# Kernel tuning notes

Hardware: AMD Instinct MI355X
Metric: run time of the kernel (lower is better)

The kernel has to match this reference:

```python
import jax, jax.numpy as jnp
import numpy as np

N, D, K = 50000, 512, 32  # n_nodes, dim_in, max neighbors (padded ragged edge_dict)


def setup_inputs() -> dict:
    key = jax.random.key(0)
    k1, k2, k3, k4, k5, k6, k7 = jax.random.split(key, 7)
    feats = jax.random.normal(k1, (N, D), dtype=jnp.float32)
    neighbors = jax.random.randint(k2, (N, K), 0, N)          # padded neighbor ids
    deg = jax.random.randint(k3, (N,), 0, K + 1)               # valid neighbor count (0 == leaf node branch)
    s = 1.0 / np.sqrt(D)  # torch nn.Linear default init range
    wq_w = jax.random.uniform(k4, (D,), jnp.float32, -s, s)
    wq_b = jax.random.uniform(k5, (), jnp.float32, -s, s)
    wk_w = jax.random.uniform(k6, (D,), jnp.float32, -s, s)
    wk_b = jax.random.uniform(k7, (), jnp.float32, -s, s)
    return dict(feats=feats, wq_w=wq_w, wq_b=wq_b, wk_w=wk_w, wk_b=wk_b,
                neighbors=neighbors, deg=deg)


def reference(feats, wq_w, wq_b, wk_w, wk_b, neighbors, deg):
    # Faithful to the original: feats is updated IN PLACE node-by-node, so later
    # nodes read already-updated neighbor features -> sequential lax.scan.
    arange_k = jnp.arange(neighbors.shape[1])
    NEG = jnp.float32(-1e9)

    def step(f, inp):
        i, nbr, d = inp
        mask = (arange_k < d).astype(f.dtype)      # [K] valid-neighbor mask
        nb = f[nbr]                                 # [K, D] neighbor gather
        ei = jnp.dot(f[i], wq_w) + wq_b             # scalar: w_q(center)
        ej = nb @ wk_w + wk_b                       # [K]:    w_k(neighbors)
        eij = ei * ej
        a = jax.nn.softmax(jnp.where(mask > 0, eij, NEG)) * mask  # softmax over dim 0
        upd = a @ nb                                # [D] weighted sum (zero when deg==0)
        new = f[i] + upd                            # in-place add_ on center row
        f = f.at[i].set(new)
        return f, new

    _, rows = jax.lax.scan(step, feats, (jnp.arange(feats.shape[0]), neighbors, deg))
    # Original returns torch.LongTensor(edge_feats) (a lossy int cast of the updated
    # rows); we return the float rows, which carry the actual computed math.
    return rows
```

## Files before the change

kernel.cpp:

```cpp
#include <hip/hip_runtime.h>


constexpr int NN = 50000;
constexpr int D  = 512;
constexpr int K  = 32;
constexpr int D4 = D / 4;

typedef float v4f __attribute__((ext_vector_type(4)));

__device__ __forceinline__ void store_f4_llc(float* p, float4 v) {
    v4f vv; vv.x = v.x; vv.y = v.y; vv.z = v.z; vv.w = v.w;
    asm volatile("global_store_dwordx4 %0, %1, off sc0 sc1"
                 :: "v"(p), "v"(vv) : "memory");
}

__global__ __launch_bounds__(256) void precomp_kernel(
    const float* __restrict__ feats,
    const float* __restrict__ wq_w, const float* __restrict__ wq_b,
    const float* __restrict__ wk_w, const float* __restrict__ wk_b,
    float* __restrict__ ei, float* __restrict__ ej_orig)
{
    int gw   = (int)((blockIdx.x * blockDim.x + threadIdx.x) >> 6);
    int lane = threadIdx.x & 63;
    if (gw >= NN) return;
    const float4* row = (const float4*)feats + (size_t)gw * D4;
    const float4* q4  = (const float4*)wq_w;
    const float4* k4  = (const float4*)wk_w;
    float dq = 0.f, dk = 0.f;
#pragma unroll
    for (int c = 0; c < 2; ++c) {
        float4 v  = row[lane + 64 * c];
        float4 q  = q4[lane + 64 * c];
        float4 kk = k4[lane + 64 * c];
        dq += v.x * q.x + v.y * q.y + v.z * q.z + v.w * q.w;
        dk += v.x * kk.x + v.y * kk.y + v.z * kk.z + v.w * kk.w;
    }
#pragma unroll
    for (int off = 32; off > 0; off >>= 1) {
        dq += __shfl_down(dq, off, 64);
        dk += __shfl_down(dk, off, 64);
    }
    if (lane == 0) {
        ei[gw]      = dq + wq_b[0];
        ej_orig[gw] = dk + wk_b[0];
    }
}

__global__ __launch_bounds__(256, 4) void attn_dataflow(
    const float* __restrict__ feats,
    const int* __restrict__ neighbors, const int* __restrict__ deg,
    const float* __restrict__ ei_arr, const float* __restrict__ ej_orig,
    const float* __restrict__ wk_w, const float* __restrict__ wk_b,
    int* ej_new,
    float* out)
{
    const int lane   = threadIdx.x & 63;
    const int gwave  = (int)((blockIdx.x * blockDim.x + threadIdx.x) >> 6);
    const int nwaves = (int)((gridDim.x * blockDim.x) >> 6);
    const float4* f4  = (const float4*)feats;
    const float4* o4r = (const float4*)out;
    const float4* wk4 = (const float4*)wk_w;
    const float   wkb = wk_b[0];

    for (int id = gwave; id < NN; id += nwaves) {
        const int d = deg[id];
        int nbr = 0;
        if (lane < K) nbr = neighbors[(size_t)id * K + lane];
        const bool valid = lane < d;
        const bool isdep = valid && (nbr < id);

        const float4 c0 = f4[(size_t)id * D4 + lane];
        const float4 c1 = f4[(size_t)id * D4 + lane + 64];
        const float eii = ei_arr[id];

        float eij = 0.f;
        if (valid && !isdep) eij = eii * ej_orig[nbr];

        float4 acc0 = {0.f, 0.f, 0.f, 0.f};
        float4 acc1 = {0.f, 0.f, 0.f, 0.f};
        float m = -3.0e38f, s = 0.f;

        unsigned long long pend = __ballot(valid && !isdep);
        unsigned long long wait = __ballot(isdep);

        while (pend | wait) {
            if (!pend) {
                int pv = 0;
                const bool w = (wait >> lane) & 1ULL;
                if (w) pv = __hip_atomic_load(&ej_new[nbr], __ATOMIC_RELAXED,
                                              __HIP_MEMORY_SCOPE_AGENT);
                unsigned long long ready = __ballot(w && pv != 0);
                if (!ready) { __builtin_amdgcn_s_sleep(1); continue; }
                if (w && pv != 0) eij = eii * __int_as_float(pv);
                pend = ready;
                wait &= ~ready;
            }
            int cnt = 0;
            int   js[4]; float ee[4];
#pragma unroll
            for (int t = 0; t < 4; ++t) {
                if (pend) {
                    int k = (int)__ffsll(pend) - 1;
                    pend &= pend - 1;
                    ee[cnt] = __shfl(eij, k, 64);
                    js[cnt] = __shfl(nbr, k, 64);
                    ++cnt;
                }
            }
            float4 v0[4], v1[4];
#pragma unroll
            for (int t = 0; t < 4; ++t) {
                if (t < cnt) {
                    const float4* sp = (js[t] < id) ? (o4r + (size_t)js[t] * D4)
                                                    : (f4  + (size_t)js[t] * D4);
                    v0[t] = sp[lane];
                    v1[t] = sp[lane + 64];
                }
            }
            float mb = m;
#pragma unroll
            for (int t = 0; t < 4; ++t) if (t < cnt) mb = fmaxf(mb, ee[t]);
            if (mb > m) {
                const float r = __expf(m - mb);
                acc0.x *= r; acc0.y *= r; acc0.z *= r; acc0.w *= r;
                acc1.x *= r; acc1.y *= r; acc1.z *= r; acc1.w *= r;
                s *= r; m = mb;
            }
#pragma unroll
            for (int t = 0; t < 4; ++t) {
                if (t < cnt) {
                    const float wt = __expf(ee[t] - m);
                    s += wt;
                    acc0.x += wt * v0[t].x; acc0.y += wt * v0[t].y;
                    acc0.z += wt * v0[t].z; acc0.w += wt * v0[t].w;
                    acc1.x += wt * v1[t].x; acc1.y += wt * v1[t].y;
                    acc1.z += wt * v1[t].z; acc1.w += wt * v1[t].w;
                }
            }
        }

        const float inv_s = (s > 0.f) ? (1.0f / s) : 0.f;
        float4 g0 = {c0.x + acc0.x * inv_s, c0.y + acc0.y * inv_s,
                     c0.z + acc0.z * inv_s, c0.w + acc0.w * inv_s};
        float4 g1 = {c1.x + acc1.x * inv_s, c1.y + acc1.y * inv_s,
                     c1.z + acc1.z * inv_s, c1.w + acc1.w * inv_s};
        float* orow = out + (size_t)id * D;
        store_f4_llc(orow + 4 * lane,        g0);
        store_f4_llc(orow + 4 * (lane + 64), g1);

        float4 w0 = wk4[lane], w1 = wk4[lane + 64];
        float pd = g0.x * w0.x + g0.y * w0.y + g0.z * w0.z + g0.w * w0.w
                 + g1.x * w1.x + g1.y * w1.y + g1.z * w1.z + g1.w * w1.w;
#pragma unroll
        for (int off = 32; off > 0; off >>= 1)
            pd += __shfl_xor(pd, off, 64);

        int bits = __float_as_int(pd + wkb);
        if (bits == 0) bits = 1;

        __builtin_amdgcn_s_waitcnt(0);
        if (lane == 0)
            __hip_atomic_store(&ej_new[id], bits,
                               __ATOMIC_RELAXED, __HIP_MEMORY_SCOPE_AGENT);
    }
}

extern "C" void kernel_launch(void* const* d_in, const int* in_sizes, int n_in,
                              void* d_out, int out_size, void* d_ws, size_t ws_size,
                              hipStream_t stream)
{
    const float* feats     = (const float*)d_in[0];
    const float* wq_w      = (const float*)d_in[1];
    const float* wq_b      = (const float*)d_in[2];
    const float* wk_w      = (const float*)d_in[3];
    const float* wk_b      = (const float*)d_in[4];
    const int*   neighbors = (const int*)d_in[5];
    const int*   deg       = (const int*)d_in[6];
    float*       out       = (float*)d_out;

    char*  ws      = (char*)d_ws;
    int*   ej_new  = (int*)ws;
    float* ei      = (float*)(ws + (size_t)(NN + 128) * sizeof(int));
    float* ej_orig = ei + NN;

    (void)hipMemsetAsync(d_ws, 0, (size_t)(NN + 128) * sizeof(int), stream);

    dim3 pb(256), pg((NN + 3) / 4);
    precomp_kernel<<<pg, pb, 0, stream>>>(feats, wq_w, wq_b, wk_w, wk_b, ei, ej_orig);

    attn_dataflow<<<dim3(1024), dim3(256), 0, stream>>>(
        feats, neighbors, deg, ei, ej_orig, wk_w, wk_b, ej_new, out);
}
```

Before: 427.9 us.

## Fuse projection precompute into dataflow kernel with per-node readiness flags

Drops the separate precompute kernel. Each wave first computes the q/k projections for its own nodes, then publishes the k projection through a flag array that consumers poll, just as they already poll updated neighbors. This removes the kernel boundary and the grid-wide wait between precompute and the sequential attention pass, so the two stages can overlap. It also doubles the grid and raises the occupancy hint to 8 blocks per CU. In exchange, every neighbor now needs a polling step, and correctness depends on all 2048 blocks being resident at once to avoid spin-wait deadlock.

After: 568.4 us. +32.8%, slower.

```diff
diff --git a/kernel.cpp b/kernel.cpp
--- a/kernel.cpp
+++ b/kernel.cpp
@@ -14,44 +14,12 @@
                  :: "v"(p), "v"(vv) : "memory");
 }
 
-__global__ __launch_bounds__(256) void precomp_kernel(
+__global__ __launch_bounds__(256, 8) void attn_dataflow(
     const float* __restrict__ feats,
+    const int* __restrict__ neighbors, const int* __restrict__ deg,
     const float* __restrict__ wq_w, const float* __restrict__ wq_b,
     const float* __restrict__ wk_w, const float* __restrict__ wk_b,
-    float* __restrict__ ei, float* __restrict__ ej_orig)
-{
-    int gw   = (int)((blockIdx.x * blockDim.x + threadIdx.x) >> 6);
-    int lane = threadIdx.x & 63;
-    if (gw >= NN) return;
-    const float4* row = (const float4*)feats + (size_t)gw * D4;
-    const float4* q4  = (const float4*)wq_w;
-    const float4* k4  = (const float4*)wk_w;
-    float dq = 0.f, dk = 0.f;
-#pragma unroll
-    for (int c = 0; c < 2; ++c) {
-        float4 v  = row[lane + 64 * c];
-        float4 q  = q4[lane + 64 * c];
-        float4 kk = k4[lane + 64 * c];
-        dq += v.x * q.x + v.y * q.y + v.z * q.z + v.w * q.w;
-        dk += v.x * kk.x + v.y * kk.y + v.z * kk.z + v.w * kk.w;
-    }
-#pragma unroll
-    for (int off = 32; off > 0; off >>= 1) {
-        dq += __shfl_down(dq, off, 64);
-        dk += __shfl_down(dk, off, 64);
-    }
-    if (lane == 0) {
-        ei[gw]      = dq + wq_b[0];
-        ej_orig[gw] = dk + wk_b[0];
-    }
-}
-
-__global__ __launch_bounds__(256, 4) void attn_dataflow(
-    const float* __restrict__ feats,
-    const int* __restrict__ neighbors, const int* __restrict__ deg,
-    const float* __restrict__ ei_arr, const float* __restrict__ ej_orig,
-    const float* __restrict__ wk_w, const float* __restrict__ wk_b,
-    int* ej_new,
+    int* ej_new, int* ej_orig, float* ei_arr,
     float* out)
 {
     const int lane   = threadIdx.x & 63;
@@ -59,8 +27,33 @@
     const int nwaves = (int)((gridDim.x * blockDim.x) >> 6);
     const float4* f4  = (const float4*)feats;
     const float4* o4r = (const float4*)out;
+    const float4* wq4 = (const float4*)wq_w;
     const float4* wk4 = (const float4*)wk_w;
+    const float   wqb = wq_b[0];
     const float   wkb = wk_b[0];
+
+    for (int id = gwave; id < NN; id += nwaves) {
+        const float4* row = f4 + (size_t)id * D4;
+        float4 v0 = row[lane],      v1 = row[lane + 64];
+        float4 q0 = wq4[lane],      q1 = wq4[lane + 64];
+        float4 k0 = wk4[lane],      k1 = wk4[lane + 64];
+        float dq = v0.x*q0.x + v0.y*q0.y + v0.z*q0.z + v0.w*q0.w
+                 + v1.x*q1.x + v1.y*q1.y + v1.z*q1.z + v1.w*q1.w;
+        float dk = v0.x*k0.x + v0.y*k0.y + v0.z*k0.z + v0.w*k0.w
+                 + v1.x*k1.x + v1.y*k1.y + v1.z*k1.z + v1.w*k1.w;
+#pragma unroll
+        for (int off = 32; off > 0; off >>= 1) {
+            dq += __shfl_down(dq, off, 64);
+            dk += __shfl_down(dk, off, 64);
+        }
+        if (lane == 0) {
+            ei_arr[id] = dq + wqb;
+            int b = __float_as_int(dk + wkb);
+            if (b == 0) b = 1;
+            __hip_atomic_store(&ej_orig[id], b,
+                               __ATOMIC_RELAXED, __HIP_MEMORY_SCOPE_AGENT);
+        }
+    }
 
     for (int id = gwave; id < NN; id += nwaves) {
         const int d = deg[id];
@@ -68,26 +61,25 @@
         if (lane < K) nbr = neighbors[(size_t)id * K + lane];
         const bool valid = lane < d;
         const bool isdep = valid && (nbr < id);
+        const int* watch = isdep ? ej_new : ej_orig;
 
         const float4 c0 = f4[(size_t)id * D4 + lane];
         const float4 c1 = f4[(size_t)id * D4 + lane + 64];
         const float eii = ei_arr[id];
 
         float eij = 0.f;
-        if (valid && !isdep) eij = eii * ej_orig[nbr];
-
         float4 acc0 = {0.f, 0.f, 0.f, 0.f};
         float4 acc1 = {0.f, 0.f, 0.f, 0.f};
         float m = -3.0e38f, s = 0.f;
 
-        unsigned long long pend = __ballot(valid && !isdep);
-        unsigned long long wait = __ballot(isdep);
+        unsigned long long pend = 0;
+        unsigned long long wait = __ballot(valid);
 
         while (pend | wait) {
             if (!pend) {
                 int pv = 0;
                 const bool w = (wait >> lane) & 1ULL;
-                if (w) pv = __hip_atomic_load(&ej_new[nbr], __ATOMIC_RELAXED,
+                if (w) pv = __hip_atomic_load(&watch[nbr], __ATOMIC_RELAXED,
                                               __HIP_MEMORY_SCOPE_AGENT);
                 unsigned long long ready = __ballot(w && pv != 0);
                 if (!ready) { __builtin_amdgcn_s_sleep(1); continue; }
@@ -180,14 +172,11 @@
 
     char*  ws      = (char*)d_ws;
     int*   ej_new  = (int*)ws;
-    float* ei      = (float*)(ws + (size_t)(NN + 128) * sizeof(int));
-    float* ej_orig = ei + NN;
+    int*   ej_orig = ej_new + NN + 64;
+    float* ei      = (float*)(ej_orig + NN + 64);
 
-    (void)hipMemsetAsync(d_ws, 0, (size_t)(NN + 128) * sizeof(int), stream);
+    (void)hipMemsetAsync(d_ws, 0, (size_t)(2 * NN + 128) * sizeof(int), stream);
 
-    dim3 pb(256), pg((NN + 3) / 4);
-    precomp_kernel<<<pg, pb, 0, stream>>>(feats, wq_w, wq_b, wk_w, wk_b, ei, ej_orig);
-
-    attn_dataflow<<<dim3(1024), dim3(256), 0, stream>>>(
-        feats, neighbors, deg, ei, ej_orig, wk_w, wk_b, ej_new, out);
+    attn_dataflow<<<dim3(2048), dim3(256), 0, stream>>>(
+        feats, neighbors, deg, wq_w, wq_b, wk_w, wk_b, ej_new, ej_orig, ei, out);
 }
```

## Gather neighbor rows from fp16 shadow copies and batch eight neighbors per step

Applied to the files above, without the earlier changes.

The precompute kernel now also writes an fp16 copy of the input features. The main kernel keeps an fp16 shadow of each updated output row alongside the fp32 output. Neighbor gathers read these half-precision rows, which halves the bytes moved on the dependent critical path, and the batch size grows from four to eight neighbors per loop iteration with padded lanes. This costs accuracy in the weighted sum and an extra 100MB of workspace writes, and falls back to the fp32 path when the workspace is too small.

New measurement: 366.8 us. 14.3% less time.

```diff
diff --git a/kernel.cpp b/kernel.cpp
--- a/kernel.cpp
+++ b/kernel.cpp
@@ -1,24 +1,40 @@
 #include <hip/hip_runtime.h>
-
-
-constexpr int NN = 50000;
-constexpr int D  = 512;
-constexpr int K  = 32;
-constexpr int D4 = D / 4;
-
-typedef float v4f __attribute__((ext_vector_type(4)));
+#include <hip/hip_fp16.h>
+
+
+constexpr int NN   = 50000;
+constexpr int D    = 512;
+constexpr int K    = 32;
+constexpr int D4   = D / 4;
+constexpr int DU16 = D / 2;
+
+typedef float        v4f __attribute__((ext_vector_type(4)));
+typedef unsigned int v4u __attribute__((ext_vector_type(4)));
 
 __device__ __forceinline__ void store_f4_llc(float* p, float4 v) {
     v4f vv; vv.x = v.x; vv.y = v.y; vv.z = v.z; vv.w = v.w;
     asm volatile("global_store_dwordx4 %0, %1, off sc0 sc1"
                  :: "v"(p), "v"(vv) : "memory");
 }
+__device__ __forceinline__ void store_u4_llc(unsigned int* p, v4u v) {
+    asm volatile("global_store_dwordx4 %0, %1, off sc0 sc1"
+                 :: "v"(p), "v"(v) : "memory");
+}
+__device__ __forceinline__ unsigned int packh2(float a, float b) {
+    __half2 h = __floats2half2_rn(a, b);
+    return *reinterpret_cast<unsigned int*>(&h);
+}
+__device__ __forceinline__ float2 unpackh2(unsigned int u) {
+    __half2 h = *reinterpret_cast<__half2*>(&u);
+    return __half22float2(h);
+}
 
 __global__ __launch_bounds__(256) void precomp_kernel(
     const float* __restrict__ feats,
     const float* __restrict__ wq_w, const float* __restrict__ wq_b,
     const float* __restrict__ wk_w, const float* __restrict__ wk_b,
-    float* __restrict__ ei, float* __restrict__ ej_orig)
+    float* __restrict__ ei, float* __restrict__ ej_orig,
+    unsigned int* __restrict__ feats16)
 {
     int gw   = (int)((blockIdx.x * blockDim.x + threadIdx.x) >> 6);
     int lane = threadIdx.x & 63;
@@ -26,33 +42,156 @@
     const float4* row = (const float4*)feats + (size_t)gw * D4;
     const float4* q4  = (const float4*)wq_w;
     const float4* k4  = (const float4*)wk_w;
-    float dq = 0.f, dk = 0.f;
-#pragma unroll
-    for (int c = 0; c < 2; ++c) {
-        float4 v  = row[lane + 64 * c];
-        float4 q  = q4[lane + 64 * c];
-        float4 kk = k4[lane + 64 * c];
-        dq += v.x * q.x + v.y * q.y + v.z * q.z + v.w * q.w;
-        dk += v.x * kk.x + v.y * kk.y + v.z * kk.z + v.w * kk.w;
-    }
+    float4 v0 = row[2 * lane], v1 = row[2 * lane + 1];
+    float4 q0 = q4[2 * lane],  q1 = q4[2 * lane + 1];
+    float4 k0 = k4[2 * lane],  k1 = k4[2 * lane + 1];
+    float dq = v0.x*q0.x + v0.y*q0.y + v0.z*q0.z + v0.w*q0.w
+             + v1.x*q1.x + v1.y*q1.y + v1.z*q1.z + v1.w*q1.w;
+    float dk = v0.x*k0.x + v0.y*k0.y + v0.z*k0.z + v0.w*k0.w
+             + v1.x*k1.x + v1.y*k1.y + v1.z*k1.z + v1.w*k1.w;
 #pragma unroll
     for (int off = 32; off > 0; off >>= 1) {
         dq += __shfl_down(dq, off, 64);
         dk += __shfl_down(dk, off, 64);
     }
+    if (feats16) {
+        v4u p;
+        p.x = packh2(v0.x, v0.y); p.y = packh2(v0.z, v0.w);
+        p.z = packh2(v1.x, v1.y); p.w = packh2(v1.z, v1.w);
+        *(v4u*)(feats16 + (size_t)gw * DU16 + 4 * lane) = p;
+    }
     if (lane == 0) {
         ei[gw]      = dq + wq_b[0];
         ej_orig[gw] = dk + wk_b[0];
     }
 }
 
-__global__ __launch_bounds__(256, 4) void attn_dataflow(
+__global__ __launch_bounds__(256, 4) void attn_dataflow_h16(
     const float* __restrict__ feats,
     const int* __restrict__ neighbors, const int* __restrict__ deg,
     const float* __restrict__ ei_arr, const float* __restrict__ ej_orig,
     const float* __restrict__ wk_w, const float* __restrict__ wk_b,
-    int* ej_new,
-    float* out)
+    const unsigned int* __restrict__ feats16, unsigned int* __restrict__ out16,
+    int* ej_new, float* out)
+{
+    const int lane   = threadIdx.x & 63;
+    const int gwave  = (int)((blockIdx.x * blockDim.x + threadIdx.x) >> 6);
+    const int nwaves = (int)((gridDim.x * blockDim.x) >> 6);
+    const float4* f4  = (const float4*)feats;
+    const float4* wk4 = (const float4*)wk_w;
+    const float   wkb = wk_b[0];
+
+    for (int id = gwave; id < NN; id += nwaves) {
+        const int d = deg[id];
+        int nbr = 0;
+        if (lane < K) nbr = neighbors[(size_t)id * K + lane];
+        const bool valid = lane < d;
+        const bool isdep = valid && (nbr < id);
+
+        const float4 c0 = f4[(size_t)id * D4 + 2 * lane];
+        const float4 c1 = f4[(size_t)id * D4 + 2 * lane + 1];
+        const float eii = ei_arr[id];
+
+        float eij = 0.f;
+        if (valid && !isdep) eij = eii * ej_orig[nbr];
+
+        float4 acc0 = {0.f, 0.f, 0.f, 0.f};
+        float4 acc1 = {0.f, 0.f, 0.f, 0.f};
+        float m = -3.0e38f, s = 0.f;
+
+        unsigned long long pend = __ballot(valid && !isdep);
+        unsigned long long wait = __ballot(isdep);
+
+        while (pend | wait) {
+            if (!pend) {
+                int pv = 0;
+                const bool w = (wait >> lane) & 1ULL;
+                if (w) pv = __hip_atomic_load(&ej_new[nbr], __ATOMIC_RELAXED,
+                                              __HIP_MEMORY_SCOPE_AGENT);
+                unsigned long long ready = __ballot(w && pv != 0);
+                if (!ready) { __builtin_amdgcn_s_sleep(1); continue; }
+                if (w && pv != 0) eij = eii * __int_as_float(pv);
+                pend = ready;
+                wait &= ~ready;
+            }
+            int js_[8]; float ee[8]; int klast = 0;
+#pragma unroll
+            for (int t = 0; t < 8; ++t) {
+                const bool has = (pend != 0);
+                int k = has ? ((int)__ffsll(pend) - 1) : klast;
+                if (has) pend &= pend - 1;
+                klast = k;
+                float ev = __shfl(eij, k, 64);
+                ee[t] = has ? ev : -3.0e38f;
+                js_[t] = __shfl(nbr, k, 64);
+            }
+            v4u pv8[8];
+#pragma unroll
+            for (int t = 0; t < 8; ++t) {
+                const unsigned int* sp = ((js_[t] < id) ? out16 : feats16)
+                                         + (size_t)js_[t] * DU16 + 4 * lane;
+                pv8[t] = *(const v4u*)sp;
+            }
+            float mb = m;
+#pragma unroll
+            for (int t = 0; t < 8; ++t) mb = fmaxf(mb, ee[t]);
+            if (mb > m) {
+                const float r = __expf(m - mb);
+                acc0.x *= r; acc0.y *= r; acc0.z *= r; acc0.w *= r;
+                acc1.x *= r; acc1.y *= r; acc1.z *= r; acc1.w *= r;
+                s *= r; m = mb;
+            }
+#pragma unroll
+            for (int t = 0; t < 8; ++t) {
+                const float wt = __expf(ee[t] - m);
+                s += wt;
+                float2 f0 = unpackh2(pv8[t].x), f1 = unpackh2(pv8[t].y);
+                float2 f2 = unpackh2(pv8[t].z), f3 = unpackh2(pv8[t].w);
+                acc0.x += wt * f0.x; acc0.y += wt * f0.y;
+                acc0.z += wt * f1.x; acc0.w += wt * f1.y;
+                acc1.x += wt * f2.x; acc1.y += wt * f2.y;
+                acc1.z += wt * f3.x; acc1.w += wt * f3.y;
+            }
+        }
+
+        const float inv_s = (s > 0.f) ? (1.0f / s) : 0.f;
+        float4 g0 = {c0.x + acc0.x * inv_s, c0.y + acc0.y * inv_s,
+                     c0.z + acc0.z * inv_s, c0.w + acc0.w * inv_s};
+        float4 g1 = {c1.x + acc1.x * inv_s, c1.y + acc1.y * inv_s,
+                     c1.z + acc1.z * inv_s, c1.w + acc1.w * inv_s};
+
+        float4* orow4 = (float4*)out + (size_t)id * D4;
+        orow4[2 * lane]     = g0;
+        orow4[2 * lane + 1] = g1;
+
+        v4u pg;
+        pg.x = packh2(g0.x, g0.y); pg.y = packh2(g0.z, g0.w);
+        pg.z = packh2(g1.x, g1.y); pg.w = packh2(g1.z, g1.w);
+        store_u4_llc(out16 + (size_t)id * DU16 + 4 * lane, pg);
+
+        float4 w0 = wk4[2 * lane], w1 = wk4[2 * lane + 1];
+        float pd = g0.x * w0.x + g0.y * w0.y + g0.z * w0.z + g0.w * w0.w
+                 + g1.x * w1.x + g1.y * w1.y + g1.z * w1.z + g1.w * w1.w;
+#pragma unroll
+        for (int off = 32; off > 0; off >>= 1)
+            pd += __shfl_xor(pd, off, 64);
+
+        int bits = __float_as_int(pd + wkb);
+        if (bits == 0) bits = 1;
+
+        __builtin_amdgcn_s_waitcnt(0);
+        if (lane == 0)
+            __hip_atomic_store(&ej_new[id], bits,
+                               __ATOMIC_RELAXED, __HIP_MEMORY_SCOPE_AGENT);
+    }
+}
+
+__global__ __launch_bounds__(256, 4) void attn_dataflow_f32(
+    const float* __restrict__ feats,
+    const int* __restrict__ neighbors, const int* __restrict__ deg,
+    const float* __restrict__ ei_arr, const float* __restrict__ ej_orig,
+    const float* __restrict__ wk_w, const float* __restrict__ wk_b,
+    int* ej_new, float* out)
 {
     const int lane   = threadIdx.x & 63;
     const int gwave  = (int)((blockIdx.x * blockDim.x + threadIdx.x) >> 6);
@@ -180,14 +319,27 @@
 
     char*  ws      = (char*)d_ws;
     int*   ej_new  = (int*)ws;
-    float* ei      = (float*)(ws + (size_t)(NN + 128) * sizeof(int));
+    float* ei      = (float*)(ej_new + NN + 64);
     float* ej_orig = ei + NN;
-
-    (void)hipMemsetAsync(d_ws, 0, (size_t)(NN + 128) * sizeof(int), stream);
+    size_t scal_end = (size_t)((char*)(ej_orig + NN) - ws);
+    size_t f16_off  = (scal_end + 1023) & ~(size_t)1023;
+    size_t f16_need = 2ull * NN * DU16 * sizeof(unsigned int);
+    const bool use16 = (ws_size >= f16_off + f16_need);
+    unsigned int* feats16 = (unsigned int*)(ws + f16_off);
+    unsigned int* out16   = feats16 + (size_t)NN * DU16;
+
+    (void)hipMemsetAsync(d_ws, 0, (size_t)NN * sizeof(int), stream);
 
     dim3 pb(256), pg((NN + 3) / 4);
-    precomp_kernel<<<pg, pb, 0, stream>>>(feats, wq_w, wq_b, wk_w, wk_b, ei, ej_orig);
-
-    attn_dataflow<<<dim3(1024), dim3(256), 0, stream>>>(
-        feats, neighbors, deg, ei, ej_orig, wk_w, wk_b, ej_new, out);
-}
+    precomp_kernel<<<pg, pb, 0, stream>>>(feats, wq_w, wq_b, wk_w, wk_b,
+                                          ei, ej_orig, use16 ? feats16 : nullptr);
+
+    if (use16) {
+        attn_dataflow_h16<<<dim3(1024), dim3(256), 0, stream>>>(
+            feats, neighbors, deg, ei, ej_orig, wk_w, wk_b,
+            feats16, out16, ej_new, out);
+    } else {
+        attn_dataflow_f32<<<dim3(1024), dim3(256), 0, stream>>>(
+            feats, neighbors, deg, ei, ej_orig, wk_w, wk_b, ej_new, out);
+    }
+}
```
